# Optimization experiments

Hardware: AMD Instinct MI355X
Metric: run time of the kernel (lower is better)

The kernel has to match this reference:

```python
import jax, jax.numpy as jnp
import numpy as np

IN_FEATS = 16
OUT_FEATS = 16
EDGE_FEATS = 16
N_NODES = 50000
N_EDGES = 800000


def setup_inputs() -> dict:
    key = jax.random.key(0)
    k = jax.random.split(key, 7)
    feat = jax.random.normal(k[0], (N_NODES, IN_FEATS), dtype=jnp.float32)
    efeat = jax.random.normal(k[1], (N_EDGES, EDGE_FEATS), dtype=jnp.float32)
    # edge_nn = Linear(EDGE_FEATS, IN_FEATS*OUT_FEATS)
    We = jax.random.normal(k[2], (EDGE_FEATS, IN_FEATS * OUT_FEATS), dtype=jnp.float32) * 0.1
    be = jax.random.normal(k[3], (IN_FEATS * OUT_FEATS,), dtype=jnp.float32) * 0.1
    bias = jax.random.normal(k[4], (OUT_FEATS,), dtype=jnp.float32) * 0.1
    src = jax.random.randint(k[5], (N_EDGES,), 0, N_NODES, dtype=jnp.int64 if jax.config.jax_enable_x64 else jnp.int32)
    dst = jnp.sort(jax.random.randint(k[6], (N_EDGES,), 0, N_NODES, dtype=jnp.int64 if jax.config.jax_enable_x64 else jnp.int32))
    return {"feat": feat, "efeat": efeat, "We": We, "be": be, "bias": bias,
            "src": src, "dst": dst, "num_nodes": N_NODES}


def reference(feat, efeat, We, be, bias, src, dst, num_nodes):
    # edge-conditioned weights: [E, in, out]
    w = (efeat @ We + be).reshape(-1, IN_FEATS, OUT_FEATS)
    # gather source features and per-edge matvec: sum_i h_src[e,i] * w[e,i,o]
    m = jnp.einsum('ei,eio->eo', feat[src], w)  # [E, out]
    # segment-sum aggregation to destination nodes ('sum' reducer)
    neigh = jax.ops.segment_sum(m, dst, num_segments=num_nodes)  # [N, out]
    # residual (Identity since in_feats == out_feats) + bias
    return neigh + feat + bias
```

## Files before the change

kernel.cpp:

```cpp
#include <hip/hip_runtime.h>
#include <hip/hip_bf16.h>

typedef __attribute__((ext_vector_type(2))) _Float16 half2v;
typedef __attribute__((ext_vector_type(8))) _Float16 half8v;
typedef __attribute__((ext_vector_type(4))) float f32x4;

#define NBLK 2048

__global__ __launch_bounds__(256) void setup_kernel(
    const float* __restrict__ feat, const float* __restrict__ bias,
    const float* __restrict__ We, const float* __restrict__ be,
    float* __restrict__ out, unsigned short* __restrict__ wp,
    int n_elems, int initB) {
  if ((int)blockIdx.x < initB) {
    int g = blockIdx.x * 256 + threadIdx.x;
    int base = g * 4;
    if (base < n_elems) {
      float4 f = *reinterpret_cast<const float4*>(feat + base);
      const float4* b4 = reinterpret_cast<const float4*>(bias);
      float4 b = b4[g & 3];
      float4 o;
      o.x = f.x + b.x; o.y = f.y + b.y; o.z = f.z + b.z; o.w = f.w + b.w;
      *reinterpret_cast<float4*>(out + base) = o;
    }
  } else {
    int idx = (blockIdx.x - initB) * 256 + threadIdx.x;
    if (idx < 9 * 4 * 16 * 8) {
      int j = idx & 7, n = (idx >> 3) & 15, gg = (idx >> 7) & 3, t = idx >> 9;
      float v = 0.f;
      if (t < 8) {
        int c = (gg >> 1) * 8 + t;
        int i = (gg & 1) * 8 + j;
        v = We[c * 256 + i * 16 + n];
      } else if (gg < 2) {
        v = be[(gg * 8 + j) * 16 + n];
      }
      _Float16 hv = (_Float16)v;
      wp[idx] = __builtin_bit_cast(unsigned short, hv);
    }
  }
}

__device__ __forceinline__ void compute_tile(
    float4 E0, float4 E1, float4 H0, float4 H1, int4 dd,
    int g, int m, const half8v* Bf, float* __restrict__ out) {
  half2v ef2[4], h2[4];
  ef2[0] = half2v{(_Float16)E0.x, (_Float16)E0.y};
  ef2[1] = half2v{(_Float16)E0.z, (_Float16)E0.w};
  ef2[2] = half2v{(_Float16)E1.x, (_Float16)E1.y};
  ef2[3] = half2v{(_Float16)E1.z, (_Float16)E1.w};
  h2[0]  = half2v{(_Float16)H0.x, (_Float16)H0.y};
  h2[1]  = half2v{(_Float16)H0.z, (_Float16)H0.w};
  h2[2]  = half2v{(_Float16)H1.x, (_Float16)H1.y};
  h2[3]  = half2v{(_Float16)H1.z, (_Float16)H1.w};

  f32x4 accA = {0.f, 0.f, 0.f, 0.f};
  f32x4 accB = {0.f, 0.f, 0.f, 0.f};
#pragma unroll
  for (int t = 0; t < 8; ++t) {
    _Float16 ev = ef2[t >> 1][t & 1];
    half2v evb = half2v{ev, ev};
    half2v a0 = evb * h2[0], a1 = evb * h2[1], a2 = evb * h2[2], a3 = evb * h2[3];
    half8v A;
    A[0] = a0[0]; A[1] = a0[1]; A[2] = a1[0]; A[3] = a1[1];
    A[4] = a2[0]; A[5] = a2[1]; A[6] = a3[0]; A[7] = a3[1];
    if (t & 1)
      accB = __builtin_amdgcn_mfma_f32_16x16x32_f16(A, Bf[t], accB, 0, 0, 0);
    else
      accA = __builtin_amdgcn_mfma_f32_16x16x32_f16(A, Bf[t], accA, 0, 0, 0);
  }
  {
    half2v z = half2v{(_Float16)0.f, (_Float16)0.f};
    half2v b0 = (g < 2) ? h2[0] : z, b1 = (g < 2) ? h2[1] : z;
    half2v b2 = (g < 2) ? h2[2] : z, b3 = (g < 2) ? h2[3] : z;
    half8v A;
    A[0] = b0[0]; A[1] = b0[1]; A[2] = b1[0]; A[3] = b1[1];
    A[4] = b2[0]; A[5] = b2[1]; A[6] = b3[0]; A[7] = b3[1];
    accB = __builtin_amdgcn_mfma_f32_16x16x32_f16(A, Bf[8], accB, 0, 0, 0);
  }
  f32x4 acc;
  acc[0] = accA[0] + accB[0]; acc[1] = accA[1] + accB[1];
  acc[2] = accA[2] + accB[2]; acc[3] = accA[3] + accB[3];

  int nA = __shfl(dd.x, 0, 64);
  int nB = __shfl(dd.w, 48, 64);
  if (nA == nB) {
    float v = acc[0] + acc[1] + acc[2] + acc[3];
    v += __shfl_xor(v, 32, 64);
    v += __shfl_xor(v, 16, 64);
    if (g == 0) unsafeAtomicAdd(out + (size_t)nA * 16 + m, v);
    return;
  }

  float run = acc[0];
  int cur = dd.x;
  if (dd.y == cur) run += acc[1];
  else { unsafeAtomicAdd(out + (size_t)cur * 16 + m, run); cur = dd.y; run = acc[1]; }
  if (dd.z == cur) run += acc[2];
  else { unsafeAtomicAdd(out + (size_t)cur * 16 + m, run); cur = dd.z; run = acc[2]; }
  if (dd.w == cur) run += acc[3];
  else { unsafeAtomicAdd(out + (size_t)cur * 16 + m, run); cur = dd.w; run = acc[3]; }
  unsafeAtomicAdd(out + (size_t)cur * 16 + m, run);
}

__global__ __launch_bounds__(256) void edge_mfma_kernel(
    const float* __restrict__ feat, const float* __restrict__ efeat,
    const int* __restrict__ src, const int* __restrict__ dst,
    const unsigned short* __restrict__ wp,
    float* __restrict__ out, int E) {
  int wid = threadIdx.x >> 6;
  int lane = threadIdx.x & 63;
  int g = lane >> 4;
  int m = lane & 15;
  int p = g >> 1;
  int hh = g & 1;

  int ntiles = (E + 15) >> 4;
  const bool partialF = (E & 15) != 0;
  const int lastT = ntiles - 1;

  int T8 = (ntiles + 7) >> 3;
  int xcd = blockIdx.x & 7;
  int wic = (blockIdx.x >> 3) * 4 + wid;
  int CW = (gridDim.x >> 3) * 4;
  int cs = xcd * T8;
  int ce = min(cs + T8, ntiles);

  int tile = cs + wic;
  if (tile >= ce) return;

  half8v Bf[9];
#pragma unroll
  for (int t = 0; t < 9; ++t)
    Bf[t] = *reinterpret_cast<const half8v*>(wp + (unsigned)(t * 64 + lane) * 8);

  const float4* ef4 = reinterpret_cast<const float4*>(efeat);
  const float4* f4  = reinterpret_cast<const float4*>(feat);
  const int4*   d4  = reinterpret_cast<const int4*>(dst);

  float4 E0, E1, H0, H1;
  int4 dd;
  if (__builtin_expect(partialF && tile == lastT, 0)) {
    int e = tile * 16 + m;
    int ec = min(e, E - 1);
    E0 = ef4[(unsigned)ec * 4 + p * 2]; E1 = ef4[(unsigned)ec * 4 + p * 2 + 1];
    if (e >= E) { E0 = make_float4(0.f,0.f,0.f,0.f); E1 = E0; }
    int s = src[ec];
    H0 = f4[(unsigned)s * 4 + hh * 2]; H1 = f4[(unsigned)s * 4 + hh * 2 + 1];
    if (e >= E) { H0 = make_float4(0.f,0.f,0.f,0.f); H1 = H0; }
    int b = tile * 16 + g * 4;
    dd.x = dst[min(b + 0, E - 1)]; dd.y = dst[min(b + 1, E - 1)];
    dd.z = dst[min(b + 2, E - 1)]; dd.w = dst[min(b + 3, E - 1)];
  } else {
    int e = tile * 16 + m;
    int s = src[e];
    E0 = ef4[(unsigned)e * 4 + p * 2]; E1 = ef4[(unsigned)e * 4 + p * 2 + 1];
    dd = d4[(unsigned)tile * 4 + g];
    H0 = f4[(unsigned)s * 4 + hh * 2]; H1 = f4[(unsigned)s * 4 + hh * 2 + 1];
  }

  int tile1 = tile + CW;
  int s1 = 0;
  if (tile1 < ce) s1 = src[min(tile1 * 16 + m, E - 1)];

  while (tile1 < ce) {
    int tile2 = tile1 + CW;

    float4 E0n, E1n, H0n, H1n;
    int4 ddn;
    if (__builtin_expect(partialF && tile1 == lastT, 0)) {
      int e = tile1 * 16 + m;
      int ec = min(e, E - 1);
      E0n = ef4[(unsigned)ec * 4 + p * 2]; E1n = ef4[(unsigned)ec * 4 + p * 2 + 1];
      if (e >= E) { E0n = make_float4(0.f,0.f,0.f,0.f); E1n = E0n; }
      int b = tile1 * 16 + g * 4;
      ddn.x = dst[min(b + 0, E - 1)]; ddn.y = dst[min(b + 1, E - 1)];
      ddn.z = dst[min(b + 2, E - 1)]; ddn.w = dst[min(b + 3, E - 1)];
    } else {
      int e = tile1 * 16 + m;
      E0n = ef4[(unsigned)e * 4 + p * 2]; E1n = ef4[(unsigned)e * 4 + p * 2 + 1];
      ddn = d4[(unsigned)tile1 * 4 + g];
    }
    H0n = f4[(unsigned)s1 * 4 + hh * 2]; H1n = f4[(unsigned)s1 * 4 + hh * 2 + 1];
    int s2 = src[min(tile2 * 16 + m, E - 1)];

    __builtin_amdgcn_sched_barrier(0);

    compute_tile(E0, E1, H0, H1, dd, g, m, Bf, out);

    E0 = E0n; E1 = E1n; H0 = H0n; H1 = H1n; dd = ddn; s1 = s2;
    tile = tile1; tile1 = tile2;
  }

  compute_tile(E0, E1, H0, H1, dd, g, m, Bf, out);
}

extern "C" void kernel_launch(void* const* d_in, const int* in_sizes, int n_in,
                              void* d_out, int out_size, void* d_ws, size_t ws_size,
                              hipStream_t stream) {
  const float* feat  = (const float*)d_in[0];
  const float* efeat = (const float*)d_in[1];
  const float* We    = (const float*)d_in[2];
  const float* be    = (const float*)d_in[3];
  const float* bias  = (const float*)d_in[4];
  const int*   src   = (const int*)d_in[5];
  const int*   dst   = (const int*)d_in[6];
  float* out = (float*)d_out;

  int E = in_sizes[5];
  int n_elems = out_size;

  int groups = (n_elems + 3) / 4;
  int initB = (groups + 255) / 256;
  int prepB = (9 * 4 * 16 * 8 + 255) / 256;
  setup_kernel<<<initB + prepB, 256, 0, stream>>>(feat, bias, We, be, out,
                                                  (unsigned short*)d_ws, n_elems, initB);

  edge_mfma_kernel<<<NBLK, 256, 0, stream>>>(feat, efeat, src, dst,
                                             (const unsigned short*)d_ws, out, E);
}
```

Baseline: 47.48 us.

## Stage edge features into LDS via async global_load_lds double buffering

Edge feature tiles are now loaded with direct global-to-LDS async loads into a per-wave double buffer with a swizzled layout, instead of going through registers as float4 loads. Each lane then reads its slice from LDS. The aim is to free VGPRs and issue contiguous 1KB tile loads, so the prefetch of the next tile overlaps compute. In exchange it adds manual vmcnt waits whose counts must match the number of outstanding loads, plus extra LDS reads, and it relies on hand-written swizzle arithmetic.

```diff
diff --git a/kernel.cpp b/kernel.cpp
--- a/kernel.cpp
+++ b/kernel.cpp
@@ -41,9 +41,33 @@
   }
 }
 
+__device__ __forceinline__ void stage_tile(const float* __restrict__ efeat,
+                                           long tile, long E, int lane,
+                                           float* lds_base ) {
+  int edge = lane >> 2;
+  int slot = (lane & 3) ^ ((lane >> 3) & 3);
+  long off = tile * 1024 + (long)edge * 64 + (long)slot * 16;
+  long mx = E * 64 - 16;
+  off = off > mx ? mx : off;
+  __builtin_amdgcn_global_load_lds(
+      (const __attribute__((address_space(1))) unsigned int*)((const char*)efeat + off),
+      (__attribute__((address_space(3))) unsigned int*)lds_base,
+      16, 0, 0);
+}
+
+__device__ __forceinline__ float4 lds_tile_read(const float* buf, int m, int h) {
+  int q = 4 * m + (h ^ ((m >> 1) & 3));
+  return *reinterpret_cast<const float4*>(buf + q * 4);
+}
+
 __device__ __forceinline__ void compute_tile(
-    float4 E0, float4 E1, float4 H0, float4 H1, int4 dd,
-    int g, int m, const half8v* Bf, float* __restrict__ out) {
+    const float* __restrict__ ebuf, float4 H0, float4 H1, int4 dd,
+    bool hvalid, int g, int m, const half8v* Bf, float* __restrict__ out) {
+  int p = g >> 1;
+  float4 E0 = lds_tile_read(ebuf, m, 2 * p);
+  float4 E1 = lds_tile_read(ebuf, m, 2 * p + 1);
+  if (!hvalid) { H0 = make_float4(0.f, 0.f, 0.f, 0.f); H1 = H0; }
+
   half2v ef2[4], h2[4];
   ef2[0] = half2v{(_Float16)E0.x, (_Float16)E0.y};
   ef2[1] = half2v{(_Float16)E0.z, (_Float16)E0.w};
@@ -91,7 +115,6 @@
     if (g == 0) unsafeAtomicAdd(out + (size_t)nA * 16 + m, v);
     return;
   }
-
   float run = acc[0];
   int cur = dd.x;
   if (dd.y == cur) run += acc[1];
@@ -108,11 +131,11 @@
     const int* __restrict__ src, const int* __restrict__ dst,
     const unsigned short* __restrict__ wp,
     float* __restrict__ out, int E) {
+  __shared__ float sbuf[4][2][256];
   int wid = threadIdx.x >> 6;
   int lane = threadIdx.x & 63;
   int g = lane >> 4;
   int m = lane & 15;
-  int p = g >> 1;
   int hh = g & 1;
 
   int ntiles = (E + 15) >> 4;
@@ -126,73 +149,60 @@
   int cs = xcd * T8;
   int ce = min(cs + T8, ntiles);
 
-  int tile = cs + wic;
-  if (tile >= ce) return;
+  int t = cs + wic;
+  if (t >= ce) return;
 
   half8v Bf[9];
 #pragma unroll
-  for (int t = 0; t < 9; ++t)
-    Bf[t] = *reinterpret_cast<const half8v*>(wp + (unsigned)(t * 64 + lane) * 8);
-
-  const float4* ef4 = reinterpret_cast<const float4*>(efeat);
-  const float4* f4  = reinterpret_cast<const float4*>(feat);
-  const int4*   d4  = reinterpret_cast<const int4*>(dst);
-
-  float4 E0, E1, H0, H1;
-  int4 dd;
-  if (__builtin_expect(partialF && tile == lastT, 0)) {
-    int e = tile * 16 + m;
-    int ec = min(e, E - 1);
-    E0 = ef4[(unsigned)ec * 4 + p * 2]; E1 = ef4[(unsigned)ec * 4 + p * 2 + 1];
-    if (e >= E) { E0 = make_float4(0.f,0.f,0.f,0.f); E1 = E0; }
-    int s = src[ec];
-    H0 = f4[(unsigned)s * 4 + hh * 2]; H1 = f4[(unsigned)s * 4 + hh * 2 + 1];
-    if (e >= E) { H0 = make_float4(0.f,0.f,0.f,0.f); H1 = H0; }
-    int b = tile * 16 + g * 4;
-    dd.x = dst[min(b + 0, E - 1)]; dd.y = dst[min(b + 1, E - 1)];
-    dd.z = dst[min(b + 2, E - 1)]; dd.w = dst[min(b + 3, E - 1)];
+  for (int tt = 0; tt < 9; ++tt)
+    Bf[tt] = *reinterpret_cast<const half8v*>(wp + (unsigned)(tt * 64 + lane) * 8);
+
+  const float4* f4 = reinterpret_cast<const float4*>(feat);
+  const int4*   d4 = reinterpret_cast<const int4*>(dst);
+
+  stage_tile(efeat, t, E, lane, &sbuf[wid][0][0]);
+  int e0 = t * 16 + m;
+  bool v_cur = e0 < E;
+  int s0 = src[min(e0, E - 1)];
+  int4 dd_cur;
+  if (__builtin_expect(partialF && t == lastT, 0)) {
+    int b = t * 16 + g * 4;
+    dd_cur.x = dst[min(b + 0, E - 1)]; dd_cur.y = dst[min(b + 1, E - 1)];
+    dd_cur.z = dst[min(b + 2, E - 1)]; dd_cur.w = dst[min(b + 3, E - 1)];
   } else {
-    int e = tile * 16 + m;
-    int s = src[e];
-    E0 = ef4[(unsigned)e * 4 + p * 2]; E1 = ef4[(unsigned)e * 4 + p * 2 + 1];
-    dd = d4[(unsigned)tile * 4 + g];
-    H0 = f4[(unsigned)s * 4 + hh * 2]; H1 = f4[(unsigned)s * 4 + hh * 2 + 1];
-  }
-
-  int tile1 = tile + CW;
-  int s1 = 0;
-  if (tile1 < ce) s1 = src[min(tile1 * 16 + m, E - 1)];
-
-  while (tile1 < ce) {
-    int tile2 = tile1 + CW;
-
-    float4 E0n, E1n, H0n, H1n;
-    int4 ddn;
-    if (__builtin_expect(partialF && tile1 == lastT, 0)) {
-      int e = tile1 * 16 + m;
-      int ec = min(e, E - 1);
-      E0n = ef4[(unsigned)ec * 4 + p * 2]; E1n = ef4[(unsigned)ec * 4 + p * 2 + 1];
-      if (e >= E) { E0n = make_float4(0.f,0.f,0.f,0.f); E1n = E0n; }
-      int b = tile1 * 16 + g * 4;
-      ddn.x = dst[min(b + 0, E - 1)]; ddn.y = dst[min(b + 1, E - 1)];
-      ddn.z = dst[min(b + 2, E - 1)]; ddn.w = dst[min(b + 3, E - 1)];
+    dd_cur = d4[(unsigned)t * 4 + g];
+  }
+  float4 H0 = f4[(unsigned)s0 * 4 + hh * 2];
+  float4 H1 = f4[(unsigned)s0 * 4 + hh * 2 + 1];
+  int t1 = t + CW;
+  int s1 = (t1 < ce) ? src[min(t1 * 16 + m, E - 1)] : 0;
+  asm volatile("s_waitcnt vmcnt(0)" ::: "memory");
+  __builtin_amdgcn_sched_barrier(0);
+
+  int buf = 0;
+  while (t1 < ce) {
+    int t2 = t1 + CW;
+    stage_tile(efeat, t1, E, lane, &sbuf[wid][buf ^ 1][0]);
+    float4 H0n = f4[(unsigned)s1 * 4 + hh * 2];
+    float4 H1n = f4[(unsigned)s1 * 4 + hh * 2 + 1];
+    int4 dd_n;
+    if (__builtin_expect(partialF && t1 == lastT, 0)) {
+      int b = t1 * 16 + g * 4;
+      dd_n.x = dst[min(b + 0, E - 1)]; dd_n.y = dst[min(b + 1, E - 1)];
+      dd_n.z = dst[min(b + 2, E - 1)]; dd_n.w = dst[min(b + 3, E - 1)];
     } else {
-      int e = tile1 * 16 + m;
-      E0n = ef4[(unsigned)e * 4 + p * 2]; E1n = ef4[(unsigned)e * 4 + p * 2 + 1];
-      ddn = d4[(unsigned)tile1 * 4 + g];
+      dd_n = d4[(unsigned)t1 * 4 + g];
     }
-    H0n = f4[(unsigned)s1 * 4 + hh * 2]; H1n = f4[(unsigned)s1 * 4 + hh * 2 + 1];
-    int s2 = src[min(tile2 * 16 + m, E - 1)];
-
+    int s2 = src[min(t2 * 16 + m, E - 1)];
+    bool v_n = (t1 * 16 + m) < E;
     __builtin_amdgcn_sched_barrier(0);
-
-    compute_tile(E0, E1, H0, H1, dd, g, m, Bf, out);
-
-    E0 = E0n; E1 = E1n; H0 = H0n; H1 = H1n; dd = ddn; s1 = s2;
-    tile = tile1; tile1 = tile2;
-  }
-
-  compute_tile(E0, E1, H0, H1, dd, g, m, Bf, out);
+    compute_tile(&sbuf[wid][buf][0], H0, H1, dd_cur, v_cur, g, m, Bf, out);
+    asm volatile("s_waitcnt vmcnt(5)" ::: "memory");
+    __builtin_amdgcn_sched_barrier(0);
+    H0 = H0n; H1 = H1n; dd_cur = dd_n; s1 = s2; v_cur = v_n;
+    t = t1; t1 = t2; buf ^= 1;
+  }
+  compute_tile(&sbuf[wid][buf][0], H0, H1, dd_cur, v_cur, g, m, Bf, out);
 }
 
 extern "C" void kernel_launch(void* const* d_in, const int* in_sizes, int n_in,
```

Result: slower. 48.58 us (+2.3%).
